# Optimization experiments

Measured on AMD Instinct MI355X. Metric: run time of the kernel, lower is better.

The kernel has to match this reference:

```python
import jax, jax.numpy as jnp
import numpy as np

LENGTH = 20
DIM = 64
BATCH = 4096
I = 16

def setup_inputs() -> dict:
    key = jax.random.key(0)
    kx, kc = jax.random.split(key)
    # binary bitstrings, values in {0,1}
    x = jax.random.randint(kx, (BATCH, I, LENGTH), 0, 2, dtype=jnp.int32)
    # embedding table of size 2^length x dim (the nn.Parameter self.cats)
    cats = jax.random.normal(kc, (2 ** LENGTH, DIM), dtype=jnp.float32)
    return {"x": x, "cats": cats}

def reference(x, cats):
    # torch.cartesian_prod orders rows so that strings[i, j] = bit j of i
    # (first column varies slowest -> weight 2^(L-1-j)).
    # The one-hot product fires where strings[i] == 1 - x, hence:
    #   idx = sum_j (1 - x_j) * 2^(L-1-j)
    L = x.shape[-1]
    weights = (jnp.int32(1) << (L - 1 - jnp.arange(L, dtype=jnp.int32)))  # (L,)
    idx = jnp.sum((1 - x) * weights, axis=-1)  # (B, I) int32 in [0, 2^L)
    # einsum of exact one-hot with cats == direct row gather
    return cats[idx]  # (B, I, D)
```

## Files before the change

kernel.cpp:

```cpp
#include <hip/hip_runtime.h>


#define BATCH 4096
#define I_DIM 16
#define LENGTH 20
#define DIM 64

#define ROWS (BATCH * I_DIM)
#define ROWS_PER_BLOCK 64
#define THREADS 256
#define PASSES ((ROWS_PER_BLOCK * (DIM / 4)) / THREADS)
#define STAGE_ITERS ((ROWS_PER_BLOCK * LENGTH) / THREADS)

typedef __attribute__((ext_vector_type(4))) float f32x4;

__global__ __launch_bounds__(THREADS) void bincat_gather(
    const int* __restrict__ x,
    const float* __restrict__ cats,
    float* __restrict__ out)
{
    __shared__ int sbits[ROWS_PER_BLOCK * LENGTH];
    __shared__ int sidx[ROWS_PER_BLOCK];

    const int t = threadIdx.x;
    const int row0 = blockIdx.x * ROWS_PER_BLOCK;

    const int base = row0 * LENGTH;
    #pragma unroll
    for (int i = 0; i < STAGE_ITERS; ++i) {
        const int k = t + i * THREADS;
        sbits[k] = __builtin_nontemporal_load(&x[base + k]);
    }
    __syncthreads();

    if (t < ROWS_PER_BLOCK) {
        int packed = 0;
        #pragma unroll
        for (int j = 0; j < LENGTH; ++j) {
            packed |= sbits[t * LENGTH + j] << (LENGTH - 1 - j);
        }
        sidx[t] = ((1 << LENGTH) - 1) ^ packed;
    }
    __syncthreads();

    const int sub = t >> 4;
    const int pos = t & 15;

    f32x4 v[PASSES];
    #pragma unroll
    for (int p = 0; p < PASSES; ++p) {
        const int r = p * 16 + sub;
        const f32x4* __restrict__ src =
            (const f32x4*)(cats + (size_t)sidx[r] * DIM);
        v[p] = src[pos];
    }

    #pragma unroll
    for (int p = 0; p < PASSES; ++p) {
        const int r = p * 16 + sub;
        f32x4* dst = (f32x4*)(out + (size_t)(row0 + r) * DIM);
        __builtin_nontemporal_store(v[p], &dst[pos]);
    }
}

extern "C" void kernel_launch(void* const* d_in, const int* in_sizes, int n_in,
                              void* d_out, int out_size, void* d_ws, size_t ws_size,
                              hipStream_t stream) {
    const int* x = (const int*)d_in[0];
    const float* cats = (const float*)d_in[1];
    float* out = (float*)d_out;

    dim3 grid(ROWS / ROWS_PER_BLOCK);
    dim3 block(THREADS);
    bincat_gather<<<grid, block, 0, stream>>>(x, cats, out);
}
```

Measured before the change: 305.3 us.

## Compute gather indices in registers via shuffles instead of shared memory

Drops the LDS staging of input bits and the two block-wide barriers. Each 16-lane group now loads its row's 20 bits as five int4 vectors and packs them into an index with an xor-shuffle reduction inside the group, so index computation proceeds per wave. The aim is to remove the serialized single-warp packing step and the barrier stalls. In exchange it adds shuffle instructions and leaves 11 of every 16 lanes idle during the x loads.

After: 307.0 us. About the same (+0.5%).

```diff
diff --git a/kernel.cpp b/kernel.cpp
--- a/kernel.cpp
+++ b/kernel.cpp
@@ -10,56 +10,48 @@
 #define ROWS_PER_BLOCK 64
 #define THREADS 256
 #define PASSES ((ROWS_PER_BLOCK * (DIM / 4)) / THREADS)
-#define STAGE_ITERS ((ROWS_PER_BLOCK * LENGTH) / THREADS)
 
 typedef __attribute__((ext_vector_type(4))) float f32x4;
+typedef __attribute__((ext_vector_type(4))) int   i32x4;
 
 __global__ __launch_bounds__(THREADS) void bincat_gather(
     const int* __restrict__ x,
     const float* __restrict__ cats,
     float* __restrict__ out)
 {
-    __shared__ int sbits[ROWS_PER_BLOCK * LENGTH];
-    __shared__ int sidx[ROWS_PER_BLOCK];
-
-    const int t = threadIdx.x;
+    const int t   = threadIdx.x;
+    const int sub = t >> 4;
+    const int pos = t & 15;
     const int row0 = blockIdx.x * ROWS_PER_BLOCK;
 
-    const int base = row0 * LENGTH;
+    int idx[PASSES];
     #pragma unroll
-    for (int i = 0; i < STAGE_ITERS; ++i) {
-        const int k = t + i * THREADS;
-        sbits[k] = __builtin_nontemporal_load(&x[base + k]);
+    for (int p = 0; p < PASSES; ++p) {
+        const int row = row0 + p * 16 + sub;
+        int partial = 0;
+        if (pos < 5) {
+            i32x4 b = __builtin_nontemporal_load(
+                (const i32x4*)(x + (size_t)row * LENGTH) + pos);
+            const int hi = 19 - 4 * pos;
+            partial = (b.x << hi) | (b.y << (hi - 1)) |
+                      (b.z << (hi - 2)) | (b.w << (hi - 3));
+        }
+        #pragma unroll
+        for (int m = 1; m < 16; m <<= 1)
+            partial |= __shfl_xor(partial, m, 16);
+        idx[p] = 0xFFFFF ^ partial;
     }
-    __syncthreads();
-
-    if (t < ROWS_PER_BLOCK) {
-        int packed = 0;
-        #pragma unroll
-        for (int j = 0; j < LENGTH; ++j) {
-            packed |= sbits[t * LENGTH + j] << (LENGTH - 1 - j);
-        }
-        sidx[t] = ((1 << LENGTH) - 1) ^ packed;
-    }
-    __syncthreads();
-
-    const int sub = t >> 4;
-    const int pos = t & 15;
 
     f32x4 v[PASSES];
     #pragma unroll
     for (int p = 0; p < PASSES; ++p) {
-        const int r = p * 16 + sub;
-        const f32x4* __restrict__ src =
-            (const f32x4*)(cats + (size_t)sidx[r] * DIM);
-        v[p] = src[pos];
+        v[p] = *((const f32x4*)(cats + (size_t)idx[p] * DIM) + pos);
     }
 
     #pragma unroll
     for (int p = 0; p < PASSES; ++p) {
-        const int r = p * 16 + sub;
-        f32x4* dst = (f32x4*)(out + (size_t)(row0 + r) * DIM);
-        __builtin_nontemporal_store(v[p], &dst[pos]);
+        f32x4* dst = (f32x4*)(out + (size_t)(row0 + p * 16 + sub) * DIM) + pos;
+        __builtin_nontemporal_store(v[p], dst);
     }
 }
 
```
